# Performance work log

Measured on AMD Instinct MI355X. Metric: run time of the kernel, lower is better.

The kernel has to match this reference:

```python
import jax, jax.numpy as jnp
import numpy as np

FEATURE_DIM = 256
HEADS = 8


def setup_inputs() -> dict:
    key = jax.random.key(0)
    ks = jax.random.split(key, 9)
    d, h = FEATURE_DIM, HEADS
    b, n = 4, 4096
    s_in = 1.0 / np.sqrt(d)
    s_out = 1.0 / np.sqrt(d * h)
    return {
        "x": jax.random.normal(ks[0], (b, n, d), dtype=jnp.float32),
        "Wq": jax.random.uniform(ks[1], (d, d * h), jnp.float32, -s_in, s_in),
        "bq": jax.random.uniform(ks[2], (d * h,), jnp.float32, -s_in, s_in),
        "Wk": jax.random.uniform(ks[3], (d, d * h), jnp.float32, -s_in, s_in),
        "bk": jax.random.uniform(ks[4], (d * h,), jnp.float32, -s_in, s_in),
        "Wv": jax.random.uniform(ks[5], (d, d * h), jnp.float32, -s_in, s_in),
        "bv": jax.random.uniform(ks[6], (d * h,), jnp.float32, -s_in, s_in),
        "Wo": jax.random.uniform(ks[7], (d * h, d), jnp.float32, -s_out, s_out),
        "bo": jax.random.uniform(ks[8], (d,), jnp.float32, -s_out, s_out),
    }


def reference(x, Wq, bq, Wk, bk, Wv, bv, Wo, bo):
    b, n, d = x.shape
    h = HEADS
    scale = d ** (-0.5)
    # projections: (b, n, h, d) -- note: NO head transpose, matching original
    q = (x @ Wq + bq).reshape(b, n, h, d)
    k = (x @ Wk + bk).reshape(b, n, h, d)
    v = (x @ Wv + bv).reshape(b, n, h, d)
    # attention is head-vs-head per token: (b, n, h, h)
    attn = jnp.einsum("bnhd,bngd->bnhg", q, k) * scale
    attn = jax.nn.softmax(attn, axis=-1)
    out = jnp.einsum("bnhg,bngd->bnhd", attn, v).reshape(b, n, h * d)
    return out @ Wo + bo
```

## Files before the change

### kernel.cpp

```cpp
#include <hip/hip_runtime.h>
#include <hip/hip_bf16.h>
#include <math.h>

typedef __bf16 bf16;
typedef __bf16 bf16x4 __attribute__((ext_vector_type(4)));
typedef __bf16 bf16x8 __attribute__((ext_vector_type(8)));
typedef float f32x4 __attribute__((ext_vector_type(4)));
typedef unsigned int u32;
typedef u32 __attribute__((address_space(1))) gu32;
typedef u32 __attribute__((address_space(3))) lu32;

#define TOK   16384
#define D_    256
#define HD    2048
#define VN    2048

#define GLDS16(g, l) __builtin_amdgcn_global_load_lds((gu32*)(g), (lu32*)(l), 16, 0, 0)
#define WAIT_LGKM0  __builtin_amdgcn_s_waitcnt(0xC07F)
#define BAR() do { __builtin_amdgcn_s_barrier(); __builtin_amdgcn_sched_barrier(0); } while (0)

__device__ __forceinline__ void transpose_body(
    const void* __restrict__ src, bf16* __restrict__ dst, int R, int C,
    int tc, int tr, int f, int mode, float (*tile)[33])
{
    int lx = threadIdx.x & 31, ly = threadIdx.x >> 5;
    for (int i = 0; i < 4; i++) {
        int r = ly + i * 8;
        size_t idx = (size_t)(tr + r) * C + tc + lx;
        tile[r][lx] = f ? ((const float*)src)[idx] : (float)((const bf16*)src)[idx];
    }
    __syncthreads();
    for (int i = 0; i < 4; i++) {
        int r = ly + i * 8;
        int k = tr + lx;
        int n = tc + r;
        size_t di;
        if (mode == 1)
            di = (size_t)n * 2048 + ((k & 255) << 3) + (k >> 8);
        else if (mode == 2)
            di = (size_t)(4096 + ((n & 255) << 3) + (n >> 8)) * 256 + k;
        else if (mode == 3)
            di = (size_t)((((n & 255) >> 4) << 8) + ((n >> 8) << 4) + (n & 15)) * 256 + k;
        else if (mode == 4)
            di = (size_t)((((n & 255) >> 4) << 8) + 128 + ((n >> 8) << 4) + (n & 15)) * 256 + k;
        else
            di = (size_t)n * R + k;
        dst[di] = (bf16)tile[lx][r];
    }
}

__global__ __launch_bounds__(256) void prep(
    const void* __restrict__ x,
    const void* __restrict__ Wq, const void* __restrict__ bq,
    const void* __restrict__ Wk, const void* __restrict__ bk,
    const void* __restrict__ Wv, const void* __restrict__ bv,
    const void* __restrict__ Wo, const void* __restrict__ bo,
    bf16* __restrict__ xb, bf16* __restrict__ WTI, bf16* __restrict__ WoT,
    bf16* __restrict__ bqkv, bf16* __restrict__ bob)
{
    __shared__ float tile[32][33];
    __shared__ int sflag;
    int tid = threadIdx.x;
    if (tid == 0) sflag = 0;
    __syncthreads();
    {
        float v = fabsf((float)((const bf16*)x)[2 * tid]);
        if (!(v < 1e4f)) sflag = 1;
    }
    __syncthreads();
    int f = sflag;
    int b = blockIdx.x;

    if (b < 4096) {
        int i = b * 256 + tid;
        bf16x4 o;
        if (f) { f32x4 v = ((const f32x4*)x)[i]; for (int e = 0; e < 4; e++) o[e] = (bf16)v[e]; }
        else   { o = ((const bf16x4*)x)[i]; }
        ((bf16x4*)xb)[i] = o;
    } else if (b < 4121) {
        int i = (b - 4096) * 256 + tid;
        if (i < 6400) {
            const void* src; bf16* dst = bqkv; int off, woff;
            if (i < 2048) {
                src = bq; off = i;
                int d = off & 255, h = off >> 8;
                woff = ((d >> 4) << 8) + (h << 4) + (d & 15);
            } else if (i < 4096) {
                src = bk; off = i - 2048;
                int d = off & 255, h = off >> 8;
                woff = ((d >> 4) << 8) + 128 + (h << 4) + (d & 15);
            } else if (i < 6144) {
                src = bv; off = i - 4096;
                woff = 4096 + ((off & 255) << 3) + (off >> 8);
            } else {
                src = bo; dst = bob; off = i - 6144; woff = off;
            }
            float v = f ? ((const float*)src)[off] : (float)((const bf16*)src)[off];
            dst[woff] = (bf16)v;
        }
        __syncthreads();
    } else if (b < 5657) {
        int idx = b - 4121;
        int tx = idx & 63, rest = idx >> 6;
        int ty = rest & 7, tz = rest >> 3;
        const void* src = (tz == 0) ? Wq : (tz == 1) ? Wk : Wv;
        int mode = (tz == 0) ? 3 : (tz == 1) ? 4 : 2;
        transpose_body(src, WTI, 256, 2048, tx * 32, ty * 32, f, mode, tile);
    } else {
        int idx = b - 5657;
        int tx = idx & 7, ty = idx >> 3;
        transpose_body(Wo, WoT, 2048, 256, tx * 32, ty * 32, f, 1, tile);
    }
}

__global__ __launch_bounds__(256) void v_proj(
    const bf16* __restrict__ X, const bf16* __restrict__ WT,
    const bf16* __restrict__ bI, bf16* __restrict__ vout)
{
    __shared__ char smem[36864];
    bf16* As = (bf16*)smem;
    bf16* Bs = (bf16*)(smem + 16384);
    int m0 = blockIdx.y * 128, n0 = blockIdx.x * 128;
    int tid = threadIdx.x, wave = tid >> 6, lane = tid & 63;
    int wm = (wave >> 1) * 64, wn = (wave & 1) * 64;
    int mrow = lane & 15, quad = lane >> 4;
    int lrow8 = lane >> 3, lslot = lane & 7;

    f32x4 acc[4][4] = {};
    for (int k0 = 0; k0 < D_; k0 += 64) {
        __syncthreads();
        for (int i = 0; i < 4; i++) {
            int rbase = wave * 32 + i * 8;
            int row = rbase + lrow8;
            int gc = lslot ^ (row & 7);
            GLDS16(&X[(size_t)(m0 + row) * D_ + k0 + gc * 8], &As[rbase * 64]);
            GLDS16(&WT[(size_t)(n0 + row) * D_ + k0 + gc * 8], &Bs[rbase * 64]);
        }
        __syncthreads();
        for (int kk = 0; kk < 64; kk += 32) {
            int slot = (((kk >> 3) + quad) ^ (mrow & 7)) * 8;
            bf16x8 af[4], bfv[4];
            for (int mt = 0; mt < 4; mt++)
                af[mt] = *(const bf16x8*)&As[(wm + mt * 16 + mrow) * 64 + slot];
            for (int nt = 0; nt < 4; nt++)
                bfv[nt] = *(const bf16x8*)&Bs[(wn + nt * 16 + mrow) * 64 + slot];
            for (int mt = 0; mt < 4; mt++)
                for (int nt = 0; nt < 4; nt++)
                    acc[mt][nt] = __builtin_amdgcn_mfma_f32_16x16x32_bf16(
                        bfv[nt], af[mt], acc[mt][nt], 0, 0, 0);
        }
    }

    __syncthreads();
    bf16* ep = (bf16*)smem + wave * (64 * 72);
    for (int mt = 0; mt < 4; mt++) {
        for (int nt = 0; nt < 4; nt++) {
            int col = n0 + wn + nt * 16 + quad * 4;
            bf16x4 bb = *(const bf16x4*)&bI[col];
            bf16x4 o;
            for (int r = 0; r < 4; r++) o[r] = (bf16)(acc[mt][nt][r] + (float)bb[r]);
            *(bf16x4*)&ep[(mt * 16 + mrow) * 72 + nt * 16 + quad * 4] = o;
        }
    }
    __syncthreads();
    for (int i = 0; i < 8; i++) {
        int r = i * 8 + (lane >> 3);
        int cb = (lane & 7) * 8;
        bf16x8 val = *(const bf16x8*)&ep[r * 72 + cb];
        *(bf16x8*)&vout[(size_t)(m0 + wm + r) * VN + n0 + wn + cb] = val;
    }
}

__global__ __launch_bounds__(512, 4) void qk_score(
    const bf16* __restrict__ X, const bf16* __restrict__ WTI,
    const bf16* __restrict__ bI, float* __restrict__ P)
{
    __shared__ bf16 Ws[64 * 256];
    __shared__ bf16 qkh[32 * 256];
    int tid = threadIdx.x, wave = tid >> 6, lane = tid & 63;
    int mrow = lane & 15, quad = lane >> 4;
    int wm3 = (wave >> 2) * 16, wn3 = (wave & 3) * 16;
    int h = lane >> 3, g = lane & 7;
    int hx = (h & 4) << 2, gx = (g & 4) << 2;
    int t0 = blockIdx.x * 32;

#pragma unroll
    for (int i = 0; i < 2; i++) {
        int row = i * 16 + wave * 2 + (lane >> 5);
        int sl = lane & 31;
        int gc = (sl & 24) | ((sl & 7) ^ (row & 7));
        GLDS16(&X[(size_t)(t0 + row) * 256 + gc * 8], &qkh[(i * 16 + wave * 2) * 256]);
    }
    __syncthreads();
    bf16x8 areg[8];
#pragma unroll
    for (int ks = 0; ks < 8; ks++) {
        int arow = wm3 + mrow;
        int sl = ks * 4 + quad;
        int ph = (sl & 24) | ((sl & 7) ^ (arow & 7));
        areg[ks] = *(const bf16x8*)&qkh[arow * 256 + ph * 8];
    }
    WAIT_LGKM0;
    BAR();

    float S[4] = {};

    for (int s = 0; s < 64; s++) {
        __syncthreads();
#pragma unroll
        for (int i = 0; i < 4; i++) {
            int row = (i * 8 + wave) * 2 + (lane >> 5);
            int sl = lane & 31;
            int gc = (sl & 24) | ((sl & 7) ^ (row & 7));
            GLDS16(&WTI[(size_t)(s * 64 + row) * 256 + gc * 8],
                   &Ws[(i * 8 + wave) * 512]);
        }
        __syncthreads();

        int brow = wn3 + mrow;
        bf16x8 bv[8];
#pragma unroll
        for (int ks = 0; ks < 8; ks++) {
            int sl = ks * 4 + quad;
            int ph = (sl & 24) | ((sl & 7) ^ (brow & 7));
            bv[ks] = *(const bf16x8*)&Ws[brow * 256 + ph * 8];
        }
        f32x4 acc = {};
#pragma unroll
        for (int ks = 0; ks < 8; ks++)
            acc = __builtin_amdgcn_mfma_f32_16x16x32_bf16(bv[ks], areg[ks], acc, 0, 0, 0);

        int sub = s & 3, qk = sub >> 1;
        int hh = (sub & 1) * 4 + (wave & 3);
        bf16x4 bb = *(const bf16x4*)&bI[s * 64 + wn3 + quad * 4];
        {
            int t = wm3 + mrow;
            bf16x4 o;
#pragma unroll
            for (int r = 0; r < 4; r++) o[r] = (bf16)(acc[r] + (float)bb[r]);
            int bo = (((qk << 8) + (hh << 5) + (quad << 3))
                      ^ ((t & 7) << 4)) ^ ((sub & 1) << 4);
            *(bf16x4*)((char*)qkh + t * 512 + bo) = o;
        }

        if (sub == 3) {
            WAIT_LGKM0;
            BAR();
#pragma unroll
            for (int u = 0; u < 4; u++) {
                int t = wave * 4 + u;
                int swz = (t & 7) << 4;
                const char* base = (const char*)qkh + t * 512;
                bf16x8 q0 = *(const bf16x8*)(base + ((((h << 5)) ^ hx) ^ swz));
                bf16x8 q1 = *(const bf16x8*)(base + ((((h << 5) + 16) ^ hx) ^ swz));
                bf16x8 k0 = *(const bf16x8*)(base + (256 + ((((g << 5)) ^ gx) ^ swz)));
                bf16x8 k1 = *(const bf16x8*)(base + (256 + ((((g << 5) + 16) ^ gx) ^ swz)));
                float a = 0.f;
#pragma unroll
                for (int e = 0; e < 8; e++)
                    a += (float)q0[e] * (float)k0[e] + (float)q1[e] * (float)k1[e];
                S[u] += a;
            }
            WAIT_LGKM0;
        }
    }

#pragma unroll
    for (int ti = 0; ti < 4; ti++) {
        int t = t0 + wave * 4 + ti;
        float sc = S[ti] * 0.0625f;
        float m = sc;
        for (int off = 1; off < 8; off <<= 1) m = fmaxf(m, __shfl_xor(m, off, 8));
        float p = __expf(sc - m);
        float sum = p;
        for (int off = 1; off < 8; off <<= 1) sum += __shfl_xor(sum, off, 8);
        P[(size_t)t * 64 + lane] = p / sum;
    }
}

__global__ __launch_bounds__(256) void out_fused(
    const bf16* __restrict__ vb, const bf16* __restrict__ WoT,
    const float* __restrict__ P, const bf16* __restrict__ bob,
    float* __restrict__ outp)
{
    __shared__ bf16 Bs[2][256 * 64];
    __shared__ bf16 Vs[2][32 * 64];
    int m0 = blockIdx.x * 32;
    int tid = threadIdx.x, wave = tid >> 6, lane = tid & 63;
    int wm = (wave >> 1) * 16, wn = (wave & 1) * 128;
    int mrow = lane & 15, quad = lane >> 4;
    int t = wm + mrow, ts = t & 7;
    int sl8 = lane >> 3, sl = lane & 7;

    float Pv[64];
    {
        const float* pr = P + (size_t)(m0 + t) * 64;
#pragma unroll
        for (int j = 0; j < 16; j++) {
            f32x4 v4 = *(const f32x4*)&pr[j * 4];
            Pv[4 * j + 0] = v4[0]; Pv[4 * j + 1] = v4[1];
            Pv[4 * j + 2] = v4[2]; Pv[4 * j + 3] = v4[3];
        }
    }

    f32x4 acc[8] = {};
    {
        int tt = (wave << 3) + sl8;
        GLDS16(&vb[(size_t)(m0 + tt) * VN + ((sl ^ (tt & 7)) << 3)],
               &Vs[0][wave * 512]);
#pragma unroll
        for (int i = 0; i < 8; i++) {
            int n = (wave << 6) + (i << 3) + sl8;
            GLDS16(&WoT[(size_t)n * HD + ((sl ^ (n & 7)) << 3)],
                   &Bs[0][((wave << 6) + (i << 3)) << 6]);
        }
    }

    for (int c = 0; c < 32; c++) {
        __syncthreads();
        if (c < 31) {
            int cc = c + 1, bb = cc & 1;
            int tt = (wave << 3) + sl8;
            GLDS16(&vb[(size_t)(m0 + tt) * VN + cc * 64 + ((sl ^ (tt & 7)) << 3)],
                   &Vs[bb][wave * 512]);
#pragma unroll
            for (int i = 0; i < 8; i++) {
                int n = (wave << 6) + (i << 3) + sl8;
                GLDS16(&WoT[(size_t)n * HD + cc * 64 + ((sl ^ (n & 7)) << 3)],
                       &Bs[bb][((wave << 6) + (i << 3)) << 6]);
            }
        }
        const bf16* Vb = Vs[c & 1];
        const bf16* Bb = Bs[c & 1];

        bf16x8 vf0 = *(const bf16x8*)&Vb[(t << 6) + ((quad ^ ts) << 3)];
        bf16x8 vf1 = *(const bf16x8*)&Vb[(t << 6) + (((quad + 4) ^ ts) << 3)];
        float v0f[8], v1f[8];
#pragma unroll
        for (int e = 0; e < 8; e++) { v0f[e] = (float)vf0[e]; v1f[e] = (float)vf1[e]; }
        bf16x8 af0, af1;
#pragma unroll
        for (int hh = 0; hh < 8; hh++) {
            float a0 = 0.f, a1 = 0.f;
#pragma unroll
            for (int gg = 0; gg < 8; gg++) {
                a0 += Pv[hh * 8 + gg] * v0f[gg];
                a1 += Pv[hh * 8 + gg] * v1f[gg];
            }
            af0[hh] = (bf16)a0; af1[hh] = (bf16)a1;
        }
#pragma unroll
        for (int nt = 0; nt < 8; nt++) {
            bf16x8 bv = *(const bf16x8*)&Bb[(wn + nt * 16 + mrow) * 64
                            + ((quad ^ (mrow & 7)) << 3)];
            acc[nt] = __builtin_amdgcn_mfma_f32_16x16x32_bf16(bv, af0, acc[nt], 0, 0, 0);
        }
#pragma unroll
        for (int nt = 0; nt < 8; nt++) {
            bf16x8 bv = *(const bf16x8*)&Bb[(wn + nt * 16 + mrow) * 64
                            + (((4 + quad) ^ (mrow & 7)) << 3)];
            acc[nt] = __builtin_amdgcn_mfma_f32_16x16x32_bf16(bv, af1, acc[nt], 0, 0, 0);
        }
    }

    int row = m0 + wm + mrow;
#pragma unroll
    for (int nt = 0; nt < 8; nt++) {
        int col = wn + nt * 16 + quad * 4;
        bf16x4 bb = *(const bf16x4*)&bob[col];
        f32x4 o;
        for (int r = 0; r < 4; r++) o[r] = acc[nt][r] + (float)bb[r];
        *(f32x4*)&outp[(size_t)row * D_ + col] = o;
    }
}

extern "C" void kernel_launch(void* const* d_in, const int* in_sizes, int n_in,
                              void* d_out, int out_size, void* d_ws, size_t ws_size,
                              hipStream_t stream)
{
    const void* x  = d_in[0];
    const void* Wq = d_in[1];
    const void* bq = d_in[2];
    const void* Wk = d_in[3];
    const void* bk = d_in[4];
    const void* Wv = d_in[5];
    const void* bv = d_in[6];
    const void* Wo = d_in[7];
    const void* bo = d_in[8];
    float* out = (float*)d_out;

    char* ws = (char*)d_ws;
    bf16*  vbuf = (bf16*)ws;
    bf16*  WTI  = (bf16*)(ws + 67108864);
    bf16*  WoT  = (bf16*)(ws + 70254592);
    bf16*  xb   = (bf16*)(ws + 71303168);
    bf16*  bqkv = (bf16*)(ws + 79691776);
    bf16*  bob  = (bf16*)(ws + 79704064);
    float* Pbuf = (float*)(ws + 79704576);

    prep<<<6169, 256, 0, stream>>>(x, Wq, bq, Wk, bk, Wv, bv, Wo, bo,
                                   xb, WTI, WoT, bqkv, bob);
    qk_score<<<512, 512, 0, stream>>>(xb, WTI, bqkv, Pbuf);
    v_proj<<<dim3(16, 128), 256, 0, stream>>>(xb, WTI + 4096 * 256, bqkv + 4096, vbuf);
    out_fused<<<512, 256, 0, stream>>>(vbuf, WoT, Pbuf, bob, out);
}
```

Before: 264.5 us.

## Restructure qk_score with 64-token tiles and per-wave double-buffered weight streaming

The QK score kernel now handles 64 tokens per block instead of 32, keeping four A fragments in registers so each loaded weight tile feeds four MFMAs. Each wave streams its own 16-row weight slice into a private double buffer with async global-to-LDS loads and a vmcnt wait, replacing the block-wide load-sync-compute loop. The Q/K weight and bias interleave moves to 8-dim groups, so each iteration yields full q/k chunks that are reduced every step instead of every fourth. The grid is halved, LDS use per block rises and occupancy drops, in exchange for less weight traffic and fewer barriers.

```diff
diff --git a/kernel.cpp b/kernel.cpp
--- a/kernel.cpp
+++ b/kernel.cpp
@@ -16,8 +16,10 @@
 #define VN    2048
 
 #define GLDS16(g, l) __builtin_amdgcn_global_load_lds((gu32*)(g), (lu32*)(l), 16, 0, 0)
+#define WAIT_VM(n)  __builtin_amdgcn_s_waitcnt(0x0F70 | (n))
 #define WAIT_LGKM0  __builtin_amdgcn_s_waitcnt(0xC07F)
 #define BAR() do { __builtin_amdgcn_s_barrier(); __builtin_amdgcn_sched_barrier(0); } while (0)
+#define SCHEDFENCE() __builtin_amdgcn_sched_barrier(0)
 
 __device__ __forceinline__ void transpose_body(
     const void* __restrict__ src, bf16* __restrict__ dst, int R, int C,
@@ -40,9 +42,9 @@
         else if (mode == 2)
             di = (size_t)(4096 + ((n & 255) << 3) + (n >> 8)) * 256 + k;
         else if (mode == 3)
-            di = (size_t)((((n & 255) >> 4) << 8) + ((n >> 8) << 4) + (n & 15)) * 256 + k;
+            di = (size_t)((((n & 255) >> 3) << 7) + ((n >> 8) << 3) + (n & 7)) * 256 + k;
         else if (mode == 4)
-            di = (size_t)((((n & 255) >> 4) << 8) + 128 + ((n >> 8) << 4) + (n & 15)) * 256 + k;
+            di = (size_t)((((n & 255) >> 3) << 7) + 64 + ((n >> 8) << 3) + (n & 7)) * 256 + k;
         else
             di = (size_t)n * R + k;
         dst[di] = (bf16)tile[lx][r];
@@ -84,11 +86,11 @@
             if (i < 2048) {
                 src = bq; off = i;
                 int d = off & 255, h = off >> 8;
-                woff = ((d >> 4) << 8) + (h << 4) + (d & 15);
+                woff = ((d >> 3) << 7) + (h << 3) + (d & 7);
             } else if (i < 4096) {
                 src = bk; off = i - 2048;
                 int d = off & 255, h = off >> 8;
-                woff = ((d >> 4) << 8) + 128 + (h << 4) + (d & 15);
+                woff = ((d >> 3) << 7) + 64 + (h << 3) + (d & 7);
             } else if (i < 6144) {
                 src = bv; off = i - 4096;
                 woff = 4096 + ((off & 255) << 3) + (off >> 8);
@@ -171,104 +173,110 @@
     }
 }
 
-__global__ __launch_bounds__(512, 4) void qk_score(
+__global__ __launch_bounds__(512, 2) void qk_score(
     const bf16* __restrict__ X, const bf16* __restrict__ WTI,
     const bf16* __restrict__ bI, float* __restrict__ P)
 {
-    __shared__ bf16 Ws[64 * 256];
-    __shared__ bf16 qkh[32 * 256];
+    __shared__ bf16 Ws[8][2][16 * 256];
+    __shared__ bf16 qkh[64 * 136];
     int tid = threadIdx.x, wave = tid >> 6, lane = tid & 63;
     int mrow = lane & 15, quad = lane >> 4;
-    int wm3 = (wave >> 2) * 16, wn3 = (wave & 3) * 16;
     int h = lane >> 3, g = lane & 7;
-    int hx = (h & 4) << 2, gx = (g & 4) << 2;
-    int t0 = blockIdx.x * 32;
-
-#pragma unroll
-    for (int i = 0; i < 2; i++) {
-        int row = i * 16 + wave * 2 + (lane >> 5);
+    int t0 = blockIdx.x * 64;
+    bf16* wsbase = &Ws[0][0][0];
+
+#pragma unroll
+    for (int i = 0; i < 4; i++) {
+        int row = (i * 8 + wave) * 2 + (lane >> 5);
         int sl = lane & 31;
         int gc = (sl & 24) | ((sl & 7) ^ (row & 7));
-        GLDS16(&X[(size_t)(t0 + row) * 256 + gc * 8], &qkh[(i * 16 + wave * 2) * 256]);
-    }
-    __syncthreads();
-    bf16x8 areg[8];
-#pragma unroll
-    for (int ks = 0; ks < 8; ks++) {
-        int arow = wm3 + mrow;
-        int sl = ks * 4 + quad;
-        int ph = (sl & 24) | ((sl & 7) ^ (arow & 7));
-        areg[ks] = *(const bf16x8*)&qkh[arow * 256 + ph * 8];
-    }
+        GLDS16(&X[(size_t)(t0 + row) * 256 + gc * 8], &wsbase[(i * 8 + wave) * 512]);
+    }
+    WAIT_VM(0);
+    BAR();
+    bf16x8 areg[4][8];
+#pragma unroll
+    for (int mt = 0; mt < 4; mt++)
+#pragma unroll
+        for (int ks = 0; ks < 8; ks++) {
+            int arow = mt * 16 + mrow;
+            int sl = ks * 4 + quad;
+            int ph = (sl & 24) | ((sl & 7) ^ (arow & 7));
+            areg[mt][ks] = *(const bf16x8*)&wsbase[arow * 256 + ph * 8];
+        }
     WAIT_LGKM0;
     BAR();
 
-    float S[4] = {};
-
-    for (int s = 0; s < 64; s++) {
-        __syncthreads();
-#pragma unroll
-        for (int i = 0; i < 4; i++) {
-            int row = (i * 8 + wave) * 2 + (lane >> 5);
-            int sl = lane & 31;
-            int gc = (sl & 24) | ((sl & 7) ^ (row & 7));
-            GLDS16(&WTI[(size_t)(s * 64 + row) * 256 + gc * 8],
-                   &Ws[(i * 8 + wave) * 512]);
-        }
-        __syncthreads();
-
-        int brow = wn3 + mrow;
-        bf16x8 bv[8];
+    bf16* wsw = &Ws[wave][0][0];
+    const bf16* wsrc = WTI + (size_t)(wave * 16) * 256;
+#define QK_STAGE(IT, BUF) {                                                    \
+        const bf16* s_ = wsrc + (size_t)(IT) * 32768;                          \
+        bf16* d_ = wsw + (BUF) * 4096;                                         \
+        _Pragma("unroll")                                                      \
+        for (int j = 0; j < 8; j++) {                                          \
+            int row = j * 2 + (lane >> 5);                                     \
+            int sl = lane & 31;                                                \
+            int gc = (sl & 24) | ((sl & 7) ^ (row & 7));                       \
+            GLDS16(&s_[(size_t)row * 256 + gc * 8], &d_[j * 512]);             \
+        } }
+    QK_STAGE(0, 0)
+    QK_STAGE(1, 1)
+
+    float S[8] = {};
+
+    for (int it = 0; it < 32; it++) {
+        if (it == 31) { WAIT_VM(0); } else { WAIT_VM(8); }
+        const bf16* wb = wsw + (it & 1) * 4096;
+        bf16x8 bvv[8];
 #pragma unroll
         for (int ks = 0; ks < 8; ks++) {
             int sl = ks * 4 + quad;
-            int ph = (sl & 24) | ((sl & 7) ^ (brow & 7));
-            bv[ks] = *(const bf16x8*)&Ws[brow * 256 + ph * 8];
-        }
-        f32x4 acc = {};
+            int ph = (sl & 24) | ((sl & 7) ^ (mrow & 7));
+            bvv[ks] = *(const bf16x8*)&wb[mrow * 256 + ph * 8];
+        }
+        WAIT_LGKM0;
+        SCHEDFENCE();
+        if (it < 30) QK_STAGE(it + 2, it & 1)
+
+        f32x4 acc[4] = {};
 #pragma unroll
         for (int ks = 0; ks < 8; ks++)
-            acc = __builtin_amdgcn_mfma_f32_16x16x32_bf16(bv[ks], areg[ks], acc, 0, 0, 0);
-
-        int sub = s & 3, qk = sub >> 1;
-        int hh = (sub & 1) * 4 + (wave & 3);
-        bf16x4 bb = *(const bf16x4*)&bI[s * 64 + wn3 + quad * 4];
-        {
-            int t = wm3 + mrow;
+#pragma unroll
+            for (int mt = 0; mt < 4; mt++)
+                acc[mt] = __builtin_amdgcn_mfma_f32_16x16x32_bf16(
+                    bvv[ks], areg[mt][ks], acc[mt], 0, 0, 0);
+
+        bf16x4 bb = *(const bf16x4*)&bI[it * 128 + wave * 16 + quad * 4];
+#pragma unroll
+        for (int mt = 0; mt < 4; mt++) {
+            int t = mt * 16 + mrow;
             bf16x4 o;
 #pragma unroll
-            for (int r = 0; r < 4; r++) o[r] = (bf16)(acc[r] + (float)bb[r]);
-            int bo = (((qk << 8) + (hh << 5) + (quad << 3))
-                      ^ ((t & 7) << 4)) ^ ((sub & 1) << 4);
-            *(bf16x4*)((char*)qkh + t * 512 + bo) = o;
-        }
-
-        if (sub == 3) {
-            WAIT_LGKM0;
-            BAR();
-#pragma unroll
-            for (int u = 0; u < 4; u++) {
-                int t = wave * 4 + u;
-                int swz = (t & 7) << 4;
-                const char* base = (const char*)qkh + t * 512;
-                bf16x8 q0 = *(const bf16x8*)(base + ((((h << 5)) ^ hx) ^ swz));
-                bf16x8 q1 = *(const bf16x8*)(base + ((((h << 5) + 16) ^ hx) ^ swz));
-                bf16x8 k0 = *(const bf16x8*)(base + (256 + ((((g << 5)) ^ gx) ^ swz)));
-                bf16x8 k1 = *(const bf16x8*)(base + (256 + ((((g << 5) + 16) ^ gx) ^ swz)));
-                float a = 0.f;
-#pragma unroll
-                for (int e = 0; e < 8; e++)
-                    a += (float)q0[e] * (float)k0[e] + (float)q1[e] * (float)k1[e];
-                S[u] += a;
-            }
-            WAIT_LGKM0;
-        }
-    }
-
-#pragma unroll
-    for (int ti = 0; ti < 4; ti++) {
-        int t = t0 + wave * 4 + ti;
-        float sc = S[ti] * 0.0625f;
+            for (int r = 0; r < 4; r++) o[r] = (bf16)(acc[mt][r] + (float)bb[r]);
+            *(bf16x4*)&qkh[t * 136 + wave * 16 + quad * 4] = o;
+        }
+        WAIT_LGKM0;
+        BAR();
+
+#pragma unroll
+        for (int u = 0; u < 8; u++) {
+            int t = wave * 8 + u;
+            bf16x8 qv = *(const bf16x8*)&qkh[t * 136 + h * 8];
+            bf16x8 kv = *(const bf16x8*)&qkh[t * 136 + 64 + g * 8];
+            float a = 0.f;
+#pragma unroll
+            for (int e = 0; e < 8; e++) a += (float)qv[e] * (float)kv[e];
+            S[u] += a;
+        }
+        WAIT_LGKM0;
+        BAR();
+    }
+#undef QK_STAGE
+
+#pragma unroll
+    for (int u = 0; u < 8; u++) {
+        int t = t0 + wave * 8 + u;
+        float sc = S[u] * 0.0625f;
         float m = sc;
         for (int off = 1; off < 8; off <<= 1) m = fmaxf(m, __shfl_xor(m, off, 8));
         float p = __expf(sc - m);
@@ -400,7 +408,7 @@
 
     prep<<<6169, 256, 0, stream>>>(x, Wq, bq, Wk, bk, Wv, bv, Wo, bo,
                                    xb, WTI, WoT, bqkv, bob);
-    qk_score<<<512, 512, 0, stream>>>(xb, WTI, bqkv, Pbuf);
+    qk_score<<<256, 512, 0, stream>>>(xb, WTI, bqkv, Pbuf);
     v_proj<<<dim3(16, 128), 256, 0, stream>>>(xb, WTI + 4096 * 256, bqkv + 4096, vbuf);
     out_fused<<<512, 256, 0, stream>>>(vbuf, WoT, Pbuf, bob, out);
 }
```

Measured after the change: 241.4 us. -8.7%, faster.
